# Performance work log

Hardware: AMD Instinct MI355X
Metric: run time of the kernel (lower is better)

The kernel has to match this reference:

```python
import jax, jax.numpy as jnp
import numpy as np

B = 2048       # batch
F_IN = 1024    # input feature dim
R_EMB = 1024   # rows of EmbedLinear sparse weight (new features)
NNZ_E = 65536  # nnz of embed sparse weight
F_OUT = 1024   # output dim of ExpandingLinear
NNZ_W = 131072 # nnz of main sparse weight [F_OUT, F_IN + R_EMB]
NNZ_B = 512    # nnz of sparse bias
F_MID = F_IN + R_EMB


def setup_inputs() -> dict:
    key = jax.random.key(0)
    ks = jax.random.split(key, 9)
    return {
        "x": jax.random.normal(ks[0], (B, F_IN), jnp.float32),
        "embed_rows": jax.random.randint(ks[1], (NNZ_E,), 0, R_EMB, jnp.int32),
        "embed_cols": jax.random.randint(ks[2], (NNZ_E,), 0, F_IN, jnp.int32),
        "embed_vals": jax.random.normal(ks[3], (NNZ_E,), jnp.float32) * 0.05,
        "w_rows": jax.random.randint(ks[4], (NNZ_W,), 0, F_OUT, jnp.int32),
        "w_cols": jax.random.randint(ks[5], (NNZ_W,), 0, F_MID, jnp.int32),
        "w_vals": jax.random.normal(ks[6], (NNZ_W,), jnp.float32) * 0.05,
        "bias_idx": jax.random.randint(ks[7], (NNZ_B,), 0, F_OUT, jnp.int32),
        "bias_vals": jax.random.normal(ks[8], (NNZ_B,), jnp.float32),
    }


def _spmm(rows, cols, vals, x, n_rows):
    # sparse COO [n_rows, F] @ x.T -> transposed: returns [B, n_rows]
    # (matches torch.sparse.mm(sparse_w, input.t()).t())
    g = vals[:, None] * x.T[cols]                              # [nnz, B] gather + scale
    return jax.ops.segment_sum(g, rows, num_segments=n_rows).T # scatter-add over rows


def reference(x, embed_rows, embed_cols, embed_vals,
              w_rows, w_cols, w_vals, bias_idx, bias_vals):
    # EmbedLinear.forward: sparse mm + ReLU + concat along features
    h = jax.nn.relu(_spmm(embed_rows, embed_cols, embed_vals, x, R_EMB))  # [B, R_EMB]
    x2 = jnp.concatenate([x, h], axis=1)                                   # [B, F_MID]
    # ExpandingLinear tail: sparse weight mm + densified sparse bias
    bias = jnp.zeros((F_OUT,), x.dtype).at[bias_idx].add(bias_vals)
    return _spmm(w_rows, w_cols, w_vals, x2, F_OUT) + bias[None, :]        # [B, F_OUT]
```

## Files before the change

kernel.cpp:

```cpp
#include <hip/hip_runtime.h>
#include <hip/hip_bf16.h>

#define B_SZ   2048
#define F_IN   1024
#define R_EMB  1024
#define F_OUT  1024
#define F_MID  2048
#define NNZ_E  65536
#define NNZ_W  131072
#define NNZ_B  512

typedef __bf16 bf16x8 __attribute__((ext_vector_type(8)));
typedef float  f32x4  __attribute__((ext_vector_type(4)));

__device__ inline void gload16(const void* g, void* l) {
    __builtin_amdgcn_global_load_lds(
        (const __attribute__((address_space(1))) void*)g,
        (__attribute__((address_space(3))) void*)l, 16, 0, 0);
}

__device__ inline ushort f2bf(float v) {
    __hip_bfloat16 h = __float2bfloat16(v);
    return *reinterpret_cast<ushort*>(&h);
}

__global__ void k_zero4(float4* __restrict__ p, int n) {
    int i = blockIdx.x * blockDim.x + threadIdx.x;
    if (i < n) p[i] = make_float4(0.f, 0.f, 0.f, 0.f);
}

__global__ void k_scatter_fused(const int* __restrict__ er, const int* __restrict__ ec,
                                const float* __restrict__ ev,
                                const int* __restrict__ wr_, const int* __restrict__ wc_,
                                const float* __restrict__ wv,
                                const int* __restrict__ bi, const float* __restrict__ bv,
                                float* __restrict__ Ef, float* __restrict__ Wf,
                                float* __restrict__ biasd) {
    int b = blockIdx.x, t = threadIdx.x;
    if (b < NNZ_E / 256) {
        int i = b * 256 + t;
        atomicAdd(&Ef[(size_t)er[i] * F_IN + ec[i]], ev[i]);
    } else if (b < NNZ_E / 256 + NNZ_W / 256) {
        int i = (b - NNZ_E / 256) * 256 + t;
        atomicAdd(&Wf[(size_t)wr_[i] * F_MID + wc_[i]], wv[i]);
    } else {
        int i = t;
        atomicAdd(&biasd[bi[i]], bv[i]);
        i += 256;
        atomicAdd(&biasd[bi[i]], bv[i]);
    }
}

__global__ void k_cvt_fused(const float4* __restrict__ x, ushort* __restrict__ x2,
                            const float4* __restrict__ Ef, ushort* __restrict__ Ebf,
                            const float4* __restrict__ Wf, ushort* __restrict__ Wbf) {
    int b = blockIdx.x, t = threadIdx.x;
    if (b < 2048) {
        int i = b * 256 + t;
        int row = i >> 8, c4 = i & 255;
        float4 v = x[i];
        ((ushort4*)x2)[(size_t)row * (F_MID / 4) + c4] =
            make_ushort4(f2bf(v.x), f2bf(v.y), f2bf(v.z), f2bf(v.w));
    } else if (b < 3072) {
        int i = (b - 2048) * 256 + t;
        float4 v = Ef[i];
        ((ushort4*)Ebf)[i] = make_ushort4(f2bf(v.x), f2bf(v.y), f2bf(v.z), f2bf(v.w));
    } else {
        int i = (b - 3072) * 256 + t;
        float4 v = Wf[i];
        ((ushort4*)Wbf)[i] = make_ushort4(f2bf(v.x), f2bf(v.y), f2bf(v.z), f2bf(v.w));
    }
}

__global__ __launch_bounds__(256)
void k_gemmA(const ushort* __restrict__ x2,
             const ushort* __restrict__ Ebf,
             const ushort* __restrict__ Wbf,
             const float* __restrict__ biasd,
             float* __restrict__ out,
             ushort* __restrict__ hOut)
{
    constexpr int BK = 64, NT = 16;
    __shared__ ushort lds[2][3][64 * 64];
    const int tid = threadIdx.x;
    const int w = tid >> 6, l = tid & 63;
    const int wr = w >> 1, wc = w & 1;
    const int la = l & 15;

    const int blk = blockIdx.x;
    const int sw  = (blk & 7) * 64 + (blk >> 3);
    const int m0  = (sw >> 4) * 64;
    const int n0  = (sw & 15) * 64;

    const int srow = w * 8 + (l >> 3);
    const int ldst = w * 512 + l * 8;

    f32x4 accE[2][2] = {}, accW[2][2] = {};

    #define STAGE(buf, k0)                                                      \
        _Pragma("unroll")                                                       \
        for (int i = 0; i < 2; ++i) {                                           \
            int row = i * 32 + srow;                                            \
            int scol = (k0) + ((((l & 7) ^ (row & 7))) << 3);                   \
            gload16(x2  + (size_t)(m0 + row) * F_MID + scol,                    \
                    &lds[buf][0][i * 2048 + ldst]);                             \
            gload16(Ebf + (size_t)(n0 + row) * F_IN + scol,                     \
                    &lds[buf][1][i * 2048 + ldst]);                             \
            gload16(Wbf + (size_t)(n0 + row) * F_MID + scol,                    \
                    &lds[buf][2][i * 2048 + ldst]);                             \
        }

    STAGE(0, 0);
    __syncthreads();

    for (int t = 0; t < NT; ++t) {
        const int cur = t & 1;
        if (t + 1 < NT) STAGE(cur ^ 1, (t + 1) * BK);

        const ushort* sA  = &lds[cur][0][0];
        const ushort* sBE = &lds[cur][1][0];
        const ushort* sBW = &lds[cur][2][0];
        #pragma unroll
        for (int ks = 0; ks < 2; ++ks) {
            const int k8 = ks * 4 + (l >> 4);
            bf16x8 af[2], be[2], bw[2];
            #pragma unroll
            for (int m = 0; m < 2; ++m) {
                int row = wr * 32 + m * 16 + la;
                af[m] = *(const bf16x8*)(sA + row * BK + ((k8 ^ (row & 7)) << 3));
            }
            #pragma unroll
            for (int n = 0; n < 2; ++n) {
                int row = wc * 32 + n * 16 + la;
                be[n] = *(const bf16x8*)(sBE + row * BK + ((k8 ^ (row & 7)) << 3));
                bw[n] = *(const bf16x8*)(sBW + row * BK + ((k8 ^ (row & 7)) << 3));
            }
            #pragma unroll
            for (int m = 0; m < 2; ++m)
                #pragma unroll
                for (int n = 0; n < 2; ++n) {
                    accE[m][n] = __builtin_amdgcn_mfma_f32_16x16x32_bf16(
                        af[m], be[n], accE[m][n], 0, 0, 0);
                    accW[m][n] = __builtin_amdgcn_mfma_f32_16x16x32_bf16(
                        af[m], bw[n], accW[m][n], 0, 0, 0);
                }
        }
        __syncthreads();
    }
    #undef STAGE

    const int lr = (l >> 4) * 4;
    #pragma unroll
    for (int m = 0; m < 2; ++m) {
        #pragma unroll
        for (int n = 0; n < 2; ++n) {
            const int col = n0 + wc * 32 + n * 16 + la;
            const float bv = biasd[col];
            #pragma unroll
            for (int j = 0; j < 4; ++j) {
                const int row = m0 + wr * 32 + m * 16 + lr + j;
                hOut[(size_t)row * F_MID + col] = f2bf(fmaxf(accE[m][n][j], 0.f));
                out[(size_t)row * F_OUT + col]  = accW[m][n][j] + bv;
            }
        }
    }
}

__global__ __launch_bounds__(256)
void k_gemmB(const ushort* __restrict__ x2,
             const ushort* __restrict__ Wbf,
             float* __restrict__ out)
{
    constexpr int BK = 64, NT = 16;
    __shared__ ushort lds[2][2][64 * 64];
    const int tid = threadIdx.x;
    const int w = tid >> 6, l = tid & 63;
    const int wr = w >> 1, wc = w & 1;
    const int la = l & 15;

    const int blk = blockIdx.x;
    const int sw  = (blk & 7) * 64 + (blk >> 3);
    const int m0  = (sw >> 4) * 64;
    const int n0  = (sw & 15) * 64;

    const ushort* A  = x2 + F_IN;
    const ushort* Bm = Wbf + F_IN;

    const int srow = w * 8 + (l >> 3);
    const int ldst = w * 512 + l * 8;

    f32x4 acc[2][2] = {};

    #define STAGE(buf, k0)                                                      \
        _Pragma("unroll")                                                       \
        for (int i = 0; i < 2; ++i) {                                           \
            int row = i * 32 + srow;                                            \
            int scol = (k0) + ((((l & 7) ^ (row & 7))) << 3);                   \
            gload16(A  + (size_t)(m0 + row) * F_MID + scol,                     \
                    &lds[buf][0][i * 2048 + ldst]);                             \
            gload16(Bm + (size_t)(n0 + row) * F_MID + scol,                     \
                    &lds[buf][1][i * 2048 + ldst]);                             \
        }

    STAGE(0, 0);
    __syncthreads();

    for (int t = 0; t < NT; ++t) {
        const int cur = t & 1;
        if (t + 1 < NT) STAGE(cur ^ 1, (t + 1) * BK);

        const ushort* sA = &lds[cur][0][0];
        const ushort* sB = &lds[cur][1][0];
        #pragma unroll
        for (int ks = 0; ks < 2; ++ks) {
            const int k8 = ks * 4 + (l >> 4);
            bf16x8 af[2], bg[2];
            #pragma unroll
            for (int m = 0; m < 2; ++m) {
                int row = wr * 32 + m * 16 + la;
                af[m] = *(const bf16x8*)(sA + row * BK + ((k8 ^ (row & 7)) << 3));
            }
            #pragma unroll
            for (int n = 0; n < 2; ++n) {
                int row = wc * 32 + n * 16 + la;
                bg[n] = *(const bf16x8*)(sB + row * BK + ((k8 ^ (row & 7)) << 3));
            }
            #pragma unroll
            for (int m = 0; m < 2; ++m)
                #pragma unroll
                for (int n = 0; n < 2; ++n)
                    acc[m][n] = __builtin_amdgcn_mfma_f32_16x16x32_bf16(
                        af[m], bg[n], acc[m][n], 0, 0, 0);
        }
        __syncthreads();
    }
    #undef STAGE

    const int lr = (l >> 4) * 4;
    #pragma unroll
    for (int m = 0; m < 2; ++m) {
        #pragma unroll
        for (int n = 0; n < 2; ++n) {
            const int col = n0 + wc * 32 + n * 16 + la;
            #pragma unroll
            for (int j = 0; j < 4; ++j) {
                const int row = m0 + wr * 32 + m * 16 + lr + j;
                out[(size_t)row * F_OUT + col] += acc[m][n][j];
            }
        }
    }
}

extern "C" void kernel_launch(void* const* d_in, const int* in_sizes, int n_in,
                              void* d_out, int out_size, void* d_ws, size_t ws_size,
                              hipStream_t stream) {
    const float* x          = (const float*)d_in[0];
    const int*   embed_rows = (const int*)  d_in[1];
    const int*   embed_cols = (const int*)  d_in[2];
    const float* embed_vals = (const float*)d_in[3];
    const int*   w_rows     = (const int*)  d_in[4];
    const int*   w_cols     = (const int*)  d_in[5];
    const float* w_vals     = (const float*)d_in[6];
    const int*   bias_idx   = (const int*)  d_in[7];
    const float* bias_vals  = (const float*)d_in[8];
    float* out = (float*)d_out;

    char* ws = (char*)d_ws;
    ushort* x2    = (ushort*)ws;
    float*  Wf    = (float*)(ws + (8u << 20));
    float*  Ef    = (float*)(ws + (16u << 20));
    float*  biasd = (float*)(ws + (20u << 20));
    ushort* Ebf   = (ushort*)(ws + (20u << 20) + 4096);
    ushort* Wbf   = (ushort*)(ws + (22u << 20) + 4096);

    k_zero4<<<3073, 256, 0, stream>>>((float4*)(ws + (8u << 20)), 786688);

    k_scatter_fused<<<NNZ_E / 256 + NNZ_W / 256 + 1, 256, 0, stream>>>(
        embed_rows, embed_cols, embed_vals,
        w_rows, w_cols, w_vals,
        bias_idx, bias_vals, Ef, Wf, biasd);

    k_cvt_fused<<<5120, 256, 0, stream>>>((const float4*)x, x2,
                                          (const float4*)Ef, Ebf,
                                          (const float4*)Wf, Wbf);

    k_gemmA<<<512, 256, 0, stream>>>(x2, Ebf, Wbf, biasd, out, x2 + F_IN);

    k_gemmB<<<512, 256, 0, stream>>>(x2, Wbf, out);
}
```

Measured before the change: 55.01 us.

## Scatter sparse weights directly into bf16 buffers with CAS and fuse prep kernels

```diff
diff --git a/kernel.cpp b/kernel.cpp
--- a/kernel.cpp
+++ b/kernel.cpp
@@ -24,36 +24,41 @@
     return *reinterpret_cast<ushort*>(&h);
 }
 
+__device__ inline float bf2f(ushort u) {
+    uint w = (uint)u << 16;
+    float f;
+    __builtin_memcpy(&f, &w, 4);
+    return f;
+}
+
+__device__ inline void bf16_scatter_add(ushort* addr, float val) {
+    uint* word = (uint*)((uintptr_t)addr & ~(uintptr_t)3);
+    const bool hi = ((uintptr_t)addr & 2) != 0;
+    uint old = __hip_atomic_load(word, __ATOMIC_RELAXED, __HIP_MEMORY_SCOPE_AGENT);
+    while (true) {
+        ushort cur = hi ? (ushort)(old >> 16) : (ushort)(old & 0xffffu);
+        ushort nv  = f2bf(bf2f(cur) + val);
+        uint neww  = hi ? ((old & 0x0000ffffu) | ((uint)nv << 16))
+                        : ((old & 0xffff0000u) | (uint)nv);
+        uint prev = atomicCAS(word, old, neww);
+        if (prev == old) break;
+        old = prev;
+    }
+}
+
 __global__ void k_zero4(float4* __restrict__ p, int n) {
     int i = blockIdx.x * blockDim.x + threadIdx.x;
     if (i < n) p[i] = make_float4(0.f, 0.f, 0.f, 0.f);
 }
 
-__global__ void k_scatter_fused(const int* __restrict__ er, const int* __restrict__ ec,
-                                const float* __restrict__ ev,
-                                const int* __restrict__ wr_, const int* __restrict__ wc_,
-                                const float* __restrict__ wv,
-                                const int* __restrict__ bi, const float* __restrict__ bv,
-                                float* __restrict__ Ef, float* __restrict__ Wf,
-                                float* __restrict__ biasd) {
-    int b = blockIdx.x, t = threadIdx.x;
-    if (b < NNZ_E / 256) {
-        int i = b * 256 + t;
-        atomicAdd(&Ef[(size_t)er[i] * F_IN + ec[i]], ev[i]);
-    } else if (b < NNZ_E / 256 + NNZ_W / 256) {
-        int i = (b - NNZ_E / 256) * 256 + t;
-        atomicAdd(&Wf[(size_t)wr_[i] * F_MID + wc_[i]], wv[i]);
-    } else {
-        int i = t;
-        atomicAdd(&biasd[bi[i]], bv[i]);
-        i += 256;
-        atomicAdd(&biasd[bi[i]], bv[i]);
-    }
-}
-
-__global__ void k_cvt_fused(const float4* __restrict__ x, ushort* __restrict__ x2,
-                            const float4* __restrict__ Ef, ushort* __restrict__ Ebf,
-                            const float4* __restrict__ Wf, ushort* __restrict__ Wbf) {
+__global__ void k_prep(const float4* __restrict__ x, ushort* __restrict__ x2,
+                       const int* __restrict__ er, const int* __restrict__ ec,
+                       const float* __restrict__ ev,
+                       const int* __restrict__ wr_, const int* __restrict__ wc_,
+                       const float* __restrict__ wv,
+                       const int* __restrict__ bi, const float* __restrict__ bv,
+                       ushort* __restrict__ Ebf, ushort* __restrict__ Wbf,
+                       float* __restrict__ biasd) {
     int b = blockIdx.x, t = threadIdx.x;
     if (b < 2048) {
         int i = b * 256 + t;
@@ -61,14 +66,15 @@
         float4 v = x[i];
         ((ushort4*)x2)[(size_t)row * (F_MID / 4) + c4] =
             make_ushort4(f2bf(v.x), f2bf(v.y), f2bf(v.z), f2bf(v.w));
-    } else if (b < 3072) {
+    } else if (b < 2048 + NNZ_E / 256) {
         int i = (b - 2048) * 256 + t;
-        float4 v = Ef[i];
-        ((ushort4*)Ebf)[i] = make_ushort4(f2bf(v.x), f2bf(v.y), f2bf(v.z), f2bf(v.w));
+        bf16_scatter_add(&Ebf[(size_t)er[i] * F_IN + ec[i]], ev[i]);
+    } else if (b < 2048 + NNZ_E / 256 + NNZ_W / 256) {
+        int i = (b - 2048 - NNZ_E / 256) * 256 + t;
+        bf16_scatter_add(&Wbf[(size_t)wr_[i] * F_MID + wc_[i]], wv[i]);
     } else {
-        int i = (b - 3072) * 256 + t;
-        float4 v = Wf[i];
-        ((ushort4*)Wbf)[i] = make_ushort4(f2bf(v.x), f2bf(v.y), f2bf(v.z), f2bf(v.w));
+        int i = (b - 2048 - NNZ_E / 256 - NNZ_W / 256) * 256 + t;
+        atomicAdd(&biasd[bi[i]], bv[i]);
     }
 }
 
@@ -267,22 +273,17 @@
 
     char* ws = (char*)d_ws;
     ushort* x2    = (ushort*)ws;
-    float*  Wf    = (float*)(ws + (8u << 20));
-    float*  Ef    = (float*)(ws + (16u << 20));
     float*  biasd = (float*)(ws + (20u << 20));
     ushort* Ebf   = (ushort*)(ws + (20u << 20) + 4096);
     ushort* Wbf   = (ushort*)(ws + (22u << 20) + 4096);
 
-    k_zero4<<<3073, 256, 0, stream>>>((float4*)(ws + (8u << 20)), 786688);
-
-    k_scatter_fused<<<NNZ_E / 256 + NNZ_W / 256 + 1, 256, 0, stream>>>(
+    k_zero4<<<1537, 256, 0, stream>>>((float4*)biasd, 393472);
+
+    k_prep<<<2048 + NNZ_E / 256 + NNZ_W / 256 + NNZ_B / 256, 256, 0, stream>>>(
+        (const float4*)x, x2,
         embed_rows, embed_cols, embed_vals,
         w_rows, w_cols, w_vals,
-        bias_idx, bias_vals, Ef, Wf, biasd);
-
-    k_cvt_fused<<<5120, 256, 0, stream>>>((const float4*)x, x2,
-                                          (const float4*)Ef, Ebf,
-                                          (const float4*)Wf, Wbf);
+        bias_idx, bias_vals, Ebf, Wbf, biasd);
 
     k_gemmA<<<512, 256, 0, stream>>>(x2, Ebf, Wbf, biasd, out, x2 + F_IN);
 
```

Measured after the change: 52.45 us. -4.6%, faster.
